# Kernel tuning notes

Hardware: AMD Instinct MI355X
Metric: run time of the kernel (lower is better)

## Reference

```python
import jax, jax.numpy as jnp
import numpy as np

H = 16  # num_heads
EPS = 1e-12  # F.normalize eps


def setup_inputs() -> dict:
    key = jax.random.key(0)
    ks = jax.random.split(key, 7)
    B, L, D = 2, 2048, 1024
    s = 0.02  # small init scale for numerical sanity
    return {
        "x": jax.random.normal(ks[0], (B, L, D), dtype=jnp.float32),
        "Wq": jax.random.normal(ks[1], (D, D), dtype=jnp.float32) * s,
        "Wk": jax.random.normal(ks[2], (D, D), dtype=jnp.float32) * s,
        "Wv": jax.random.normal(ks[3], (D, D), dtype=jnp.float32) * s,
        "Wo": jax.random.normal(ks[4], (D, D), dtype=jnp.float32) * s,
        "Wb": jax.random.normal(ks[5], (D, H), dtype=jnp.float32) * s,
        "bb": jnp.zeros((H,), dtype=jnp.float32),
    }


def _l2norm(t):
    # matches torch F.normalize(p=2, dim=-1): x / max(||x||, eps)
    n = jnp.sqrt(jnp.sum(t * t, axis=-1, keepdims=True))
    return t / jnp.maximum(n, EPS)


def reference(x, Wq, Wk, Wv, Wo, Wb, bb):
    B, L, Dm = x.shape
    Dh = Dm // H
    q = (x @ Wq).reshape(B, L, H, Dh)
    k = (x @ Wk).reshape(B, L, H, Dh)
    v = (x @ Wv).reshape(B, L, H, Dh)
    beta = jax.nn.sigmoid(x @ Wb + bb)  # [B, L, H]
    q = _l2norm(q)
    k = _l2norm(k)
    # out[b,l,h,e] = sum_{t<=l} beta[b,t,h] * <q[b,l,h], k[b,t,h]> * v[b,t,h,e]
    # Exact reformulation of the cumsum-of-outer-products in the source,
    # avoiding the B*L*H*Dh*Dh state blow-up.
    scores = jnp.einsum('blhd,bthd->bhlt', q, k)
    scores = scores * beta.transpose(0, 2, 1)[:, :, None, :]  # scale by beta_t
    mask = jnp.tril(jnp.ones((L, L), dtype=scores.dtype))  # causal incl. diagonal
    scores = scores * mask
    out = jnp.einsum('bhlt,bthe->blhe', scores, v).reshape(B, L, Dm)
    return out @ Wo
```

## Files before the change

### kernel.cpp

```cpp
#include <hip/hip_runtime.h>
#include <stdint.h>

#define DEV static __device__ __forceinline__

typedef __bf16 bf16x8 __attribute__((ext_vector_type(8)));
typedef unsigned short u16x8 __attribute__((ext_vector_type(8)));
typedef float f32x4 __attribute__((ext_vector_type(4)));

DEV unsigned short f2bf(float f) {
    unsigned int u = __builtin_bit_cast(unsigned int, f);
    u = (u + 0x7FFFu + ((u >> 16) & 1u)) >> 16;
    return (unsigned short)u;
}
DEV float bf2f(unsigned short h) {
    unsigned int u = ((unsigned int)h) << 16;
    return __builtin_bit_cast(float, u);
}

DEV void gload_lds16(const unsigned short* g, unsigned short* l) {
    __builtin_amdgcn_global_load_lds(
        (const __attribute__((address_space(1))) unsigned int*)g,
        (__attribute__((address_space(3))) unsigned int*)l, 16, 0, 0);
}

__global__ __launch_bounds__(256) void k_prep0(
    const float* __restrict__ x, const float* __restrict__ Wq,
    const float* __restrict__ Wk, const float* __restrict__ Wv,
    const float* __restrict__ Wo, unsigned short* __restrict__ xb,
    unsigned short* __restrict__ Wqkvt, unsigned short* __restrict__ Wot) {
    __shared__ float tile[64][65];
    int bid = blockIdx.x, tid = threadIdx.x;
    if (bid < 4096) {
        int i = bid * 256 + tid;
        float4 v = ((const float4*)x)[i];
        ushort4 o;
        o.x = f2bf(v.x); o.y = f2bf(v.y); o.z = f2bf(v.z); o.w = f2bf(v.w);
        ((ushort4*)xb)[i] = o;
    } else {
        int idx = bid - 4096;
        int z = idx >> 8, rem = idx & 255;
        const float* W = (z == 0) ? Wq : (z == 1) ? Wk : (z == 2) ? Wv : Wo;
        int k0 = (rem & 15) * 64, n0 = (rem >> 4) * 64;
        int tx = tid & 63, ty = tid >> 6;
        #pragma unroll
        for (int r = 0; r < 64; r += 4)
            tile[ty + r][tx] = W[(size_t)(k0 + ty + r) * 1024 + n0 + tx];
        __syncthreads();
        #pragma unroll
        for (int r = 0; r < 64; r += 4) {
            float v = tile[tx][ty + r];
            int n = n0 + ty + r, k = k0 + tx;
            if (z < 3) Wqkvt[(size_t)(z * 1024 + n) * 1024 + k] = f2bf(v);
            else       Wot[(size_t)n * 1024 + k] = f2bf(v);
        }
    }
}

__global__ __launch_bounds__(256) void k_beta(const float* __restrict__ x,
                                              const float* __restrict__ Wb,
                                              const float* __restrict__ bb,
                                              float* __restrict__ beta) {
    __shared__ unsigned short WbT[16 * 1024];
    int tid = threadIdx.x;
    #pragma unroll
    for (int j = 0; j < 16; j++) {
        int idx4 = tid + 256 * j;
        float4 v = ((const float4*)Wb)[idx4];
        int i = idx4 >> 2;
        int h0 = (idx4 & 3) * 4;
        WbT[(h0 + 0) * 1024 + (i ^ ((h0 + 0) << 2))] = f2bf(v.x);
        WbT[(h0 + 1) * 1024 + (i ^ ((h0 + 1) << 2))] = f2bf(v.y);
        WbT[(h0 + 2) * 1024 + (i ^ ((h0 + 2) << 2))] = f2bf(v.z);
        WbT[(h0 + 3) * 1024 + (i ^ ((h0 + 3) << 2))] = f2bf(v.w);
    }
    __syncthreads();
    int w = tid >> 6, lane = tid & 63;
    int row = blockIdx.x * 4 + w;
    const float* xr = x + (size_t)row * 1024;
    float acc[16] = {};
    #pragma unroll
    for (int k = 0; k < 16; k++) {
        int i = lane + 64 * k;
        float xv = xr[i];
        #pragma unroll
        for (int h = 0; h < 16; h++)
            acc[h] += xv * bf2f(WbT[h * 1024 + (i ^ (h << 2))]);
    }
    #pragma unroll
    for (int h = 0; h < 16; h++) {
        #pragma unroll
        for (int m = 32; m; m >>= 1) acc[h] += __shfl_xor(acc[h], m, 64);
    }
    if (lane == 0) {
        #pragma unroll
        for (int h = 0; h < 16; h++)
            beta[row * 16 + h] = 1.f / (1.f + __expf(-(acc[h] + bb[h])));
    }
}

__global__ __launch_bounds__(256) void k_gemm_qkv(const unsigned short* __restrict__ A,
                                                  const unsigned short* __restrict__ Bt,
                                                  unsigned short* __restrict__ C) {
    __shared__ unsigned short As[128 * 64];
    __shared__ unsigned short Bs[128 * 64];
    int m0 = blockIdx.x * 128, n0 = blockIdx.y * 128;
    int tid = threadIdx.x;
    int w = tid >> 6, lane = tid & 63, g = lane >> 4, ln = lane & 15;
    int wr = w >> 1, wc = w & 1;
    f32x4 acc[4][4] = {};
    for (int k0 = 0; k0 < 1024; k0 += 64) {
        #pragma unroll
        for (int cc = 0; cc < 4; cc++) {
            int base = (w * 4 + cc) * 64;
            int chunk = base + lane;
            int row = chunk >> 3, ps = chunk & 7;
            int sl = (ps - (row >> 1)) & 7;
            gload_lds16(A + (size_t)(m0 + row) * 1024 + k0 + sl * 8, &As[base * 8]);
            gload_lds16(Bt + (size_t)(n0 + row) * 1024 + k0 + sl * 8, &Bs[base * 8]);
        }
        __syncthreads();
        #pragma unroll
        for (int s = 0; s < 2; s++) {
            bf16x8 af[4], bfr[4];
            #pragma unroll
            for (int mi = 0; mi < 4; mi++) {
                int row = wr * 64 + mi * 16 + ln;
                int ps = (s * 4 + g + (row >> 1)) & 7;
                af[mi] = *(const bf16x8*)(&As[row * 64 + ps * 8]);
            }
            #pragma unroll
            for (int ni = 0; ni < 4; ni++) {
                int row = wc * 64 + ni * 16 + ln;
                int ps = (s * 4 + g + (row >> 1)) & 7;
                bfr[ni] = *(const bf16x8*)(&Bs[row * 64 + ps * 8]);
            }
            #pragma unroll
            for (int mi = 0; mi < 4; mi++)
                #pragma unroll
                for (int ni = 0; ni < 4; ni++)
                    acc[mi][ni] = __builtin_amdgcn_mfma_f32_16x16x32_bf16(
                        af[mi], bfr[ni], acc[mi][ni], 0, 0, 0);
        }
        __syncthreads();
    }
    #pragma unroll
    for (int mi = 0; mi < 4; mi++)
        #pragma unroll
        for (int ni = 0; ni < 4; ni++)
            #pragma unroll
            for (int r = 0; r < 4; r++) {
                int row = m0 + wr * 64 + mi * 16 + g * 4 + r;
                int col = n0 + wc * 64 + ni * 16 + ln;
                C[(size_t)row * 3072 + col] = f2bf(acc[mi][ni][r]);
            }
}

__global__ __launch_bounds__(256) void k_gemm_out(const unsigned short* __restrict__ A,
                                                  const unsigned short* __restrict__ Bt,
                                                  float* __restrict__ C) {
    __shared__ unsigned short As[128 * 64];
    __shared__ unsigned short Bs[64 * 64];
    int m0 = blockIdx.x * 128, n0 = blockIdx.y * 64;
    int tid = threadIdx.x;
    int w = tid >> 6, lane = tid & 63, g = lane >> 4, ln = lane & 15;
    int wr = w >> 1, wc = w & 1;
    f32x4 acc[4][2] = {};
    for (int k0 = 0; k0 < 1024; k0 += 64) {
        #pragma unroll
        for (int i = 0; i < 6; i++) {
            int base = w * 384 + i * 64;
            int chunk = base + lane;
            if (base < 1024) {
                int row = chunk >> 3, ps = chunk & 7;
                int sl = (ps - (row >> 1)) & 7;
                gload_lds16(A + (size_t)(m0 + row) * 1024 + k0 + sl * 8, &As[base * 8]);
            } else {
                int bc = chunk - 1024;
                int row = bc >> 3, ps = bc & 7;
                int sl = (ps - (row >> 1)) & 7;
                gload_lds16(Bt + (size_t)(n0 + row) * 1024 + k0 + sl * 8, &Bs[(base - 1024) * 8]);
            }
        }
        __syncthreads();
        #pragma unroll
        for (int s = 0; s < 2; s++) {
            bf16x8 af[4], bfr[2];
            #pragma unroll
            for (int mi = 0; mi < 4; mi++) {
                int row = wr * 64 + mi * 16 + ln;
                int ps = (s * 4 + g + (row >> 1)) & 7;
                af[mi] = *(const bf16x8*)(&As[row * 64 + ps * 8]);
            }
            #pragma unroll
            for (int ni = 0; ni < 2; ni++) {
                int row = wc * 32 + ni * 16 + ln;
                int ps = (s * 4 + g + (row >> 1)) & 7;
                bfr[ni] = *(const bf16x8*)(&Bs[row * 64 + ps * 8]);
            }
            #pragma unroll
            for (int mi = 0; mi < 4; mi++)
                #pragma unroll
                for (int ni = 0; ni < 2; ni++)
                    acc[mi][ni] = __builtin_amdgcn_mfma_f32_16x16x32_bf16(
                        af[mi], bfr[ni], acc[mi][ni], 0, 0, 0);
        }
        __syncthreads();
    }
    #pragma unroll
    for (int mi = 0; mi < 4; mi++)
        #pragma unroll
        for (int ni = 0; ni < 2; ni++)
            #pragma unroll
            for (int r = 0; r < 4; r++) {
                int row = m0 + wr * 64 + mi * 16 + g * 4 + r;
                int col = n0 + wc * 32 + ni * 16 + ln;
                C[(size_t)row * 1024 + col] = acc[mi][ni][r];
            }
}

DEV int vswz(int dh, int ks) { return (ks ^ (dh & 7) ^ ((dh >> 3) & 7)) & 7; }

__global__ __launch_bounds__(256) void k_state(const unsigned short* __restrict__ QKV,
                                               const float* __restrict__ beta,
                                               unsigned short* __restrict__ Mbuf) {
    __shared__ unsigned short Kt[64 * 64];
    __shared__ unsigned short Vt[64 * 64];
    int c = blockIdx.x, bh = blockIdx.y;
    int b = bh >> 4, h = bh & 15;
    int tid = threadIdx.x, w = tid >> 6, lane = tid & 63, g = lane >> 4, ln = lane & 15;
    int row0 = b * 2048 + c * 64;
    const unsigned short* Kg = QKV + 1024;
    const unsigned short* Vg = QKV + 2048;
    #pragma unroll
    for (int cc = 0; cc < 2; cc++) {
        int ci = tid + cc * 256;
        int r = ci >> 3, sl = ci & 7;
        uint4 kd = *(const uint4*)(Kg + (size_t)(row0 + r) * 3072 + h * 64 + sl * 8);
        uint4 vd = *(const uint4*)(Vg + (size_t)(row0 + r) * 3072 + h * 64 + sl * 8);
        union { uint4 q; unsigned short s[8]; } uk, uv;
        uk.q = kd; uv.q = vd;
        float ssk = 0.f;
        #pragma unroll
        for (int i = 0; i < 8; i++) { float v = bf2f(uk.s[i]); ssk += v * v; }
        ssk += __shfl_xor(ssk, 1, 64);
        ssk += __shfl_xor(ssk, 2, 64);
        ssk += __shfl_xor(ssk, 4, 64);
        float ksc = beta[(row0 + r) * 16 + h] / fmaxf(sqrtf(ssk), 1e-12f);
        #pragma unroll
        for (int i = 0; i < 8; i++) {
            int dh = sl * 8 + i;
            int off = dh * 64 + vswz(dh, r >> 3) * 8 + (r & 7);
            Kt[off] = f2bf(bf2f(uk.s[i]) * ksc);
            Vt[off] = uv.s[i];
        }
    }
    __syncthreads();
    f32x4 macc[4] = {};
    #pragma unroll
    for (int st = 0; st < 2; st++) {
        int c0 = st * 32 + g * 4;
        int rk = w * 16 + ln;
        uint2 klo = *(const uint2*)(&Kt[rk * 64 + vswz(rk, c0 >> 3) * 8 + (c0 & 7)]);
        uint2 khi = *(const uint2*)(&Kt[rk * 64 + vswz(rk, (c0 + 16) >> 3) * 8 + (c0 & 7)]);
        uint4 kc = make_uint4(klo.x, klo.y, khi.x, khi.y);
        bf16x8 bfrag = __builtin_bit_cast(bf16x8, kc);
        #pragma unroll
        for (int mt = 0; mt < 4; mt++) {
            int rv = mt * 16 + ln;
            uint2 lo = *(const uint2*)(&Vt[rv * 64 + vswz(rv, c0 >> 3) * 8 + (c0 & 7)]);
            uint2 hi = *(const uint2*)(&Vt[rv * 64 + vswz(rv, (c0 + 16) >> 3) * 8 + (c0 & 7)]);
            uint4 comb = make_uint4(lo.x, lo.y, hi.x, hi.y);
            bf16x8 afrag = __builtin_bit_cast(bf16x8, comb);
            macc[mt] = __builtin_amdgcn_mfma_f32_16x16x32_bf16(afrag, bfrag, macc[mt], 0, 0, 0);
        }
    }
    unsigned short* Mc = Mbuf + ((size_t)bh * 32 + c) * 4096;
    #pragma unroll
    for (int mt = 0; mt < 4; mt++)
        #pragma unroll
        for (int r = 0; r < 4; r++)
            Mc[(mt * 16 + g * 4 + r) * 64 + w * 16 + ln] = f2bf(macc[mt][r]);
}

__global__ __launch_bounds__(256) void k_prefix(unsigned short* __restrict__ Mbuf) {
    int bh = blockIdx.x >> 3, slice = blockIdx.x & 7;
    int base = slice * 512 + threadIdx.x * 2;
    unsigned short* M = Mbuf + (size_t)bh * 32 * 4096 + base;
    unsigned int v[32];
    #pragma unroll
    for (int c = 0; c < 32; c++) v[c] = *(const unsigned int*)(M + (size_t)c * 4096);
    float a0 = 0.f, a1 = 0.f;
    #pragma unroll
    for (int c = 0; c < 32; c++) {
        unsigned int pack = (unsigned int)f2bf(a0) | ((unsigned int)f2bf(a1) << 16);
        *(unsigned int*)(M + (size_t)c * 4096) = pack;
        a0 += bf2f((unsigned short)(v[c] & 0xFFFF));
        a1 += bf2f((unsigned short)(v[c] >> 16));
    }
}

__global__ __launch_bounds__(256) void k_attn2(const unsigned short* __restrict__ QKV,
                                               const unsigned short* __restrict__ Sbuf,
                                               const float* __restrict__ beta,
                                               unsigned short* __restrict__ attn) {
    __shared__ unsigned short Ks[64 * 64];
    __shared__ unsigned short Vt[64 * 64];
    __shared__ unsigned short STs[64 * 64];
    int qt = blockIdx.x, bh = blockIdx.y;
    int b = bh >> 4, h = bh & 15;
    int tid = threadIdx.x, w = tid >> 6, lane = tid & 63, g = lane >> 4, ln = lane & 15;
    int rowbase = b * 2048 + qt * 64;

    const unsigned short* Kg = QKV + 1024;
    const unsigned short* Vg = QKV + 2048;
    const unsigned short* Sg = Sbuf + ((size_t)bh * 32 + qt) * 4096;

    #pragma unroll
    for (int cc = 0; cc < 2; cc++) {
        int c = tid + cc * 256;
        int r = c >> 3, psl = c & 7;
        int sl = psl ^ (r & 7);
        gload_lds16(Sg + r * 64 + sl * 8, &STs[(cc * 256 + w * 64) * 8]);
    }

    const unsigned short* Qrow = QKV + (size_t)(rowbase + w * 16 + ln) * 3072 + h * 64;
    u16x8 qu0 = *(const u16x8*)(Qrow + g * 8);
    u16x8 qu1 = *(const u16x8*)(Qrow + 32 + g * 8);
    bf16x8 qf[2];
    qf[0] = __builtin_bit_cast(bf16x8, qu0);
    qf[1] = __builtin_bit_cast(bf16x8, qu1);
    float ssq = 0.f;
    #pragma unroll
    for (int j = 0; j < 8; j++) {
        float v0 = bf2f(qu0[j]), v1 = bf2f(qu1[j]);
        ssq += v0 * v0 + v1 * v1;
    }
    ssq += __shfl_xor(ssq, 16, 64);
    ssq += __shfl_xor(ssq, 32, 64);
    float qscale = 1.f / fmaxf(sqrtf(ssq), 1e-12f);

    #pragma unroll
    for (int cc = 0; cc < 2; cc++) {
        int c = tid + cc * 256;
        int r = c >> 3, sl = c & 7;
        uint4 kd = *(const uint4*)(Kg + (size_t)(rowbase + r) * 3072 + h * 64 + sl * 8);
        union { uint4 q; unsigned short s[8]; } uk; uk.q = kd;
        float ssk = 0.f;
        #pragma unroll
        for (int i = 0; i < 8; i++) { float v = bf2f(uk.s[i]); ssk += v * v; }
        ssk += __shfl_xor(ssk, 1, 64);
        ssk += __shfl_xor(ssk, 2, 64);
        ssk += __shfl_xor(ssk, 4, 64);
        float ksc = beta[(rowbase + r) * 16 + h] / fmaxf(sqrtf(ssk), 1e-12f);
        #pragma unroll
        for (int i = 0; i < 8; i++) uk.s[i] = f2bf(bf2f(uk.s[i]) * ksc);
        *(uint4*)(&Ks[r * 64 + ((sl ^ (r & 7)) * 8)]) = uk.q;
        uint4 vd = *(const uint4*)(Vg + (size_t)(rowbase + r) * 3072 + h * 64 + sl * 8);
        union { uint4 q; unsigned short s[8]; } uv; uv.q = vd;
        #pragma unroll
        for (int i = 0; i < 8; i++) {
            int dh = sl * 8 + i;
            Vt[dh * 64 + vswz(dh, r >> 3) * 8 + (r & 7)] = uv.s[i];
        }
    }
    __syncthreads();

    f32x4 oacc[4] = {};

    #pragma unroll
    for (int st = 0; st < 2; st++)
        #pragma unroll
        for (int mt2 = 0; mt2 < 4; mt2++) {
            int r = mt2 * 16 + ln;
            int ps = (st * 4 + g) ^ (r & 7);
            bf16x8 a = *(const bf16x8*)(&STs[r * 64 + ps * 8]);
            oacc[mt2] = __builtin_amdgcn_mfma_f32_16x16x32_bf16(a, qf[st], oacc[mt2], 0, 0, 0);
        }

    f32x4 s[4] = {};
    #pragma unroll
    for (int st = 0; st < 2; st++)
        #pragma unroll
        for (int mt = 0; mt < 4; mt++) {
            int r = mt * 16 + ln;
            int ps = (st * 4 + g) ^ (r & 7);
            bf16x8 a = *(const bf16x8*)(&Ks[r * 64 + ps * 8]);
            s[mt] = __builtin_amdgcn_mfma_f32_16x16x32_bf16(a, qf[st], s[mt], 0, 0, 0);
        }
    {
        int qr = w * 16 + ln;
        #pragma unroll
        for (int mt = 0; mt < 4; mt++)
            #pragma unroll
            for (int r = 0; r < 4; r++)
                if (mt * 16 + g * 4 + r > qr) s[mt][r] = 0.f;
    }
    bf16x8 pf[2];
    #pragma unroll
    for (int st = 0; st < 2; st++) {
        u16x8 t;
        #pragma unroll
        for (int r = 0; r < 4; r++) {
            t[r]     = f2bf(s[2 * st][r]);
            t[4 + r] = f2bf(s[2 * st + 1][r]);
        }
        pf[st] = __builtin_bit_cast(bf16x8, t);
    }
    #pragma unroll
    for (int st = 0; st < 2; st++)
        #pragma unroll
        for (int mt2 = 0; mt2 < 4; mt2++) {
            int rv = mt2 * 16 + ln;
            int c0 = st * 32 + g * 4;
            uint2 lo = *(const uint2*)(&Vt[rv * 64 + vswz(rv, c0 >> 3) * 8 + (c0 & 7)]);
            uint2 hi = *(const uint2*)(&Vt[rv * 64 + vswz(rv, (c0 + 16) >> 3) * 8 + (c0 & 7)]);
            uint4 comb = make_uint4(lo.x, lo.y, hi.x, hi.y);
            bf16x8 a = __builtin_bit_cast(bf16x8, comb);
            oacc[mt2] = __builtin_amdgcn_mfma_f32_16x16x32_bf16(a, pf[st], oacc[mt2], 0, 0, 0);
        }
    __syncthreads();

    {
        int qr = w * 16 + ln;
        #pragma unroll
        for (int mt2 = 0; mt2 < 4; mt2++)
            #pragma unroll
            for (int r = 0; r < 4; r++) {
                int dh = mt2 * 16 + g * 4 + r;
                Ks[qr * 64 + (dh ^ ((qr & 7) << 3))] = f2bf(oacc[mt2][r] * qscale);
            }
    }
    __syncthreads();
    #pragma unroll
    for (int cc = 0; cc < 2; cc++) {
        int c = tid + cc * 256;
        int r = c >> 3, sl = c & 7;
        uint4 d = *(const uint4*)(&Ks[r * 64 + ((sl ^ (r & 7)) * 8)]);
        *(uint4*)(attn + (size_t)(rowbase + r) * 1024 + h * 64 + sl * 8) = d;
    }
}

extern "C" void kernel_launch(void* const* d_in, const int* in_sizes, int n_in,
                              void* d_out, int out_size, void* d_ws, size_t ws_size,
                              hipStream_t stream) {
    const float* x  = (const float*)d_in[0];
    const float* Wq = (const float*)d_in[1];
    const float* Wk = (const float*)d_in[2];
    const float* Wv = (const float*)d_in[3];
    const float* Wo = (const float*)d_in[4];
    const float* Wb = (const float*)d_in[5];
    const float* bb = (const float*)d_in[6];
    float* out = (float*)d_out;

    char* ws = (char*)d_ws;
    unsigned short* xb    = (unsigned short*)(ws);
    unsigned short* Mbuf  = (unsigned short*)(ws);
    unsigned short* Wqkvt = (unsigned short*)(ws + (8ull  << 20));
    unsigned short* Wot   = (unsigned short*)(ws + (14ull << 20));
    unsigned short* QKVb  = (unsigned short*)(ws + (16ull << 20));
    float*          beta  = (float*)         (ws + (40ull << 20));
    unsigned short* attn  = (unsigned short*)(ws + (41ull << 20));

    k_prep0<<<5120, 256, 0, stream>>>(x, Wq, Wk, Wv, Wo, xb, Wqkvt, Wot);
    k_beta<<<1024, 256, 0, stream>>>(x, Wb, bb, beta);
    k_gemm_qkv<<<dim3(32, 24), 256, 0, stream>>>(xb, Wqkvt, QKVb);
    k_state<<<dim3(32, 32), 256, 0, stream>>>(QKVb, beta, Mbuf);
    k_prefix<<<256, 256, 0, stream>>>(Mbuf);
    k_attn2<<<dim3(32, 32), 256, 0, stream>>>(QKVb, Mbuf, beta, attn);
    k_gemm_out<<<dim3(32, 16), 256, 0, stream>>>(attn, Wot, out);
}
```

Baseline: 177.7 us.

## Merge beta into prep kernel and store normalized K for reuse in attention

The beta projection kernel is folded into the prep kernel as an extra range of blocks, which removes one launch and lets it run alongside the conversions. k_state now writes the beta-scaled, L2-normalized K back into the QKV buffer in place. k_attn2 then loads that K straight into LDS with async global-to-LDS copies instead of recomputing the norm and scaling. The cost is an extra global write of K in k_state and a cross-kernel data dependency on the rewritten buffer.

```diff
diff --git a/kernel.cpp b/kernel.cpp
--- a/kernel.cpp
+++ b/kernel.cpp
@@ -23,12 +23,14 @@
         (__attribute__((address_space(3))) unsigned int*)l, 16, 0, 0);
 }
 
-__global__ __launch_bounds__(256) void k_prep0(
+__global__ __launch_bounds__(256) void k_prep(
     const float* __restrict__ x, const float* __restrict__ Wq,
     const float* __restrict__ Wk, const float* __restrict__ Wv,
-    const float* __restrict__ Wo, unsigned short* __restrict__ xb,
-    unsigned short* __restrict__ Wqkvt, unsigned short* __restrict__ Wot) {
-    __shared__ float tile[64][65];
+    const float* __restrict__ Wo, const float* __restrict__ Wb,
+    const float* __restrict__ bb, unsigned short* __restrict__ xb,
+    unsigned short* __restrict__ Wqkvt, unsigned short* __restrict__ Wot,
+    float* __restrict__ beta) {
+    __shared__ __align__(16) char smem[32768];
     int bid = blockIdx.x, tid = threadIdx.x;
     if (bid < 4096) {
         int i = bid * 256 + tid;
@@ -36,7 +38,8 @@
         ushort4 o;
         o.x = f2bf(v.x); o.y = f2bf(v.y); o.z = f2bf(v.z); o.w = f2bf(v.w);
         ((ushort4*)xb)[i] = o;
-    } else {
+    } else if (bid < 5120) {
+        float (*tile)[65] = (float(*)[65])smem;
         int idx = bid - 4096;
         int z = idx >> 8, rem = idx & 255;
         const float* W = (z == 0) ? Wq : (z == 1) ? Wk : (z == 2) ? Wv : Wo;
@@ -53,48 +56,43 @@
             if (z < 3) Wqkvt[(size_t)(z * 1024 + n) * 1024 + k] = f2bf(v);
             else       Wot[(size_t)n * 1024 + k] = f2bf(v);
         }
-    }
-}
-
-__global__ __launch_bounds__(256) void k_beta(const float* __restrict__ x,
-                                              const float* __restrict__ Wb,
-                                              const float* __restrict__ bb,
-                                              float* __restrict__ beta) {
-    __shared__ unsigned short WbT[16 * 1024];
-    int tid = threadIdx.x;
-    #pragma unroll
-    for (int j = 0; j < 16; j++) {
-        int idx4 = tid + 256 * j;
-        float4 v = ((const float4*)Wb)[idx4];
-        int i = idx4 >> 2;
-        int h0 = (idx4 & 3) * 4;
-        WbT[(h0 + 0) * 1024 + (i ^ ((h0 + 0) << 2))] = f2bf(v.x);
-        WbT[(h0 + 1) * 1024 + (i ^ ((h0 + 1) << 2))] = f2bf(v.y);
-        WbT[(h0 + 2) * 1024 + (i ^ ((h0 + 2) << 2))] = f2bf(v.z);
-        WbT[(h0 + 3) * 1024 + (i ^ ((h0 + 3) << 2))] = f2bf(v.w);
-    }
-    __syncthreads();
-    int w = tid >> 6, lane = tid & 63;
-    int row = blockIdx.x * 4 + w;
-    const float* xr = x + (size_t)row * 1024;
-    float acc[16] = {};
-    #pragma unroll
-    for (int k = 0; k < 16; k++) {
-        int i = lane + 64 * k;
-        float xv = xr[i];
-        #pragma unroll
-        for (int h = 0; h < 16; h++)
-            acc[h] += xv * bf2f(WbT[h * 1024 + (i ^ (h << 2))]);
-    }
-    #pragma unroll
-    for (int h = 0; h < 16; h++) {
-        #pragma unroll
-        for (int m = 32; m; m >>= 1) acc[h] += __shfl_xor(acc[h], m, 64);
-    }
-    if (lane == 0) {
-        #pragma unroll
-        for (int h = 0; h < 16; h++)
-            beta[row * 16 + h] = 1.f / (1.f + __expf(-(acc[h] + bb[h])));
+    } else {
+        unsigned short* WbT = (unsigned short*)smem;
+        int bbl = bid - 5120;
+        #pragma unroll
+        for (int j = 0; j < 16; j++) {
+            int idx4 = tid + 256 * j;
+            float4 v = ((const float4*)Wb)[idx4];
+            int i = idx4 >> 2;
+            int h0 = (idx4 & 3) * 4;
+            WbT[(h0 + 0) * 1024 + (i ^ ((h0 + 0) << 2))] = f2bf(v.x);
+            WbT[(h0 + 1) * 1024 + (i ^ ((h0 + 1) << 2))] = f2bf(v.y);
+            WbT[(h0 + 2) * 1024 + (i ^ ((h0 + 2) << 2))] = f2bf(v.z);
+            WbT[(h0 + 3) * 1024 + (i ^ ((h0 + 3) << 2))] = f2bf(v.w);
+        }
+        __syncthreads();
+        int w = tid >> 6, lane = tid & 63;
+        int row = bbl * 4 + w;
+        const float* xr = x + (size_t)row * 1024;
+        float acc[16] = {};
+        #pragma unroll
+        for (int k = 0; k < 16; k++) {
+            int i = lane + 64 * k;
+            float xv = xr[i];
+            #pragma unroll
+            for (int h = 0; h < 16; h++)
+                acc[h] += xv * bf2f(WbT[h * 1024 + (i ^ (h << 2))]);
+        }
+        #pragma unroll
+        for (int h = 0; h < 16; h++) {
+            #pragma unroll
+            for (int m = 32; m; m >>= 1) acc[h] += __shfl_xor(acc[h], m, 64);
+        }
+        if (lane == 0) {
+            #pragma unroll
+            for (int h = 0; h < 16; h++)
+                beta[row * 16 + h] = 1.f / (1.f + __expf(-(acc[h] + bb[h])));
+        }
     }
 }
 
@@ -220,7 +218,7 @@
 
 DEV int vswz(int dh, int ks) { return (ks ^ (dh & 7) ^ ((dh >> 3) & 7)) & 7; }
 
-__global__ __launch_bounds__(256) void k_state(const unsigned short* __restrict__ QKV,
+__global__ __launch_bounds__(256) void k_state(unsigned short* __restrict__ QKV,
                                                const float* __restrict__ beta,
                                                unsigned short* __restrict__ Mbuf) {
     __shared__ unsigned short Kt[64 * 64];
@@ -229,7 +227,7 @@
     int b = bh >> 4, h = bh & 15;
     int tid = threadIdx.x, w = tid >> 6, lane = tid & 63, g = lane >> 4, ln = lane & 15;
     int row0 = b * 2048 + c * 64;
-    const unsigned short* Kg = QKV + 1024;
+    unsigned short* Kg = QKV + 1024;
     const unsigned short* Vg = QKV + 2048;
     #pragma unroll
     for (int cc = 0; cc < 2; cc++) {
@@ -247,10 +245,13 @@
         ssk += __shfl_xor(ssk, 4, 64);
         float ksc = beta[(row0 + r) * 16 + h] / fmaxf(sqrtf(ssk), 1e-12f);
         #pragma unroll
+        for (int i = 0; i < 8; i++) uk.s[i] = f2bf(bf2f(uk.s[i]) * ksc);
+        *(uint4*)(Kg + (size_t)(row0 + r) * 3072 + h * 64 + sl * 8) = uk.q;
+        #pragma unroll
         for (int i = 0; i < 8; i++) {
             int dh = sl * 8 + i;
             int off = dh * 64 + vswz(dh, r >> 3) * 8 + (r & 7);
-            Kt[off] = f2bf(bf2f(uk.s[i]) * ksc);
+            Kt[off] = uk.s[i];
             Vt[off] = uv.s[i];
         }
     }
@@ -301,7 +302,6 @@
 
 __global__ __launch_bounds__(256) void k_attn2(const unsigned short* __restrict__ QKV,
                                                const unsigned short* __restrict__ Sbuf,
-                                               const float* __restrict__ beta,
                                                unsigned short* __restrict__ attn) {
     __shared__ unsigned short Ks[64 * 64];
     __shared__ unsigned short Vt[64 * 64];
@@ -321,6 +321,8 @@
         int r = c >> 3, psl = c & 7;
         int sl = psl ^ (r & 7);
         gload_lds16(Sg + r * 64 + sl * 8, &STs[(cc * 256 + w * 64) * 8]);
+        gload_lds16(Kg + (size_t)(rowbase + r) * 3072 + h * 64 + sl * 8,
+                    &Ks[(cc * 256 + w * 64) * 8]);
     }
 
     const unsigned short* Qrow = QKV + (size_t)(rowbase + w * 16 + ln) * 3072 + h * 64;
@@ -343,18 +345,6 @@
     for (int cc = 0; cc < 2; cc++) {
         int c = tid + cc * 256;
         int r = c >> 3, sl = c & 7;
-        uint4 kd = *(const uint4*)(Kg + (size_t)(rowbase + r) * 3072 + h * 64 + sl * 8);
-        union { uint4 q; unsigned short s[8]; } uk; uk.q = kd;
-        float ssk = 0.f;
-        #pragma unroll
-        for (int i = 0; i < 8; i++) { float v = bf2f(uk.s[i]); ssk += v * v; }
-        ssk += __shfl_xor(ssk, 1, 64);
-        ssk += __shfl_xor(ssk, 2, 64);
-        ssk += __shfl_xor(ssk, 4, 64);
-        float ksc = beta[(rowbase + r) * 16 + h] / fmaxf(sqrtf(ssk), 1e-12f);
-        #pragma unroll
-        for (int i = 0; i < 8; i++) uk.s[i] = f2bf(bf2f(uk.s[i]) * ksc);
-        *(uint4*)(&Ks[r * 64 + ((sl ^ (r & 7)) * 8)]) = uk.q;
         uint4 vd = *(const uint4*)(Vg + (size_t)(rowbase + r) * 3072 + h * 64 + sl * 8);
         union { uint4 q; unsigned short s[8]; } uv; uv.q = vd;
         #pragma unroll
@@ -461,11 +451,10 @@
     float*          beta  = (float*)         (ws + (40ull << 20));
     unsigned short* attn  = (unsigned short*)(ws + (41ull << 20));
 
-    k_prep0<<<5120, 256, 0, stream>>>(x, Wq, Wk, Wv, Wo, xb, Wqkvt, Wot);
-    k_beta<<<1024, 256, 0, stream>>>(x, Wb, bb, beta);
+    k_prep<<<6144, 256, 0, stream>>>(x, Wq, Wk, Wv, Wo, Wb, bb, xb, Wqkvt, Wot, beta);
     k_gemm_qkv<<<dim3(32, 24), 256, 0, stream>>>(xb, Wqkvt, QKVb);
     k_state<<<dim3(32, 32), 256, 0, stream>>>(QKVb, beta, Mbuf);
     k_prefix<<<256, 256, 0, stream>>>(Mbuf);
-    k_attn2<<<dim3(32, 32), 256, 0, stream>>>(QKVb, Mbuf, beta, attn);
+    k_attn2<<<dim3(32, 32), 256, 0, stream>>>(QKVb, Mbuf, attn);
     k_gemm_out<<<dim3(32, 16), 256, 0, stream>>>(attn, Wot, out);
 }
```

After: 173.0 us. 2.6% less time.
